# Kernel tuning notes

Hardware: AMD Instinct MI355X
Metric: run time of the kernel (lower is better)

The kernel has to match this reference:

```python
import jax, jax.numpy as jnp
import numpy as np

B, N, DIM, H, DH = 2, 256, 512, 8, 64
CLAMP = 40.0


def rmsnorm(x, w):
    eps = jnp.finfo(x.dtype).eps
    return x * jax.lax.rsqrt(jnp.mean(x * x, axis=-1, keepdims=True) + eps) * w


def strassen_attend(q, k1, k2, v1, v2, sim_clamp_value):
    # q,k1,k2: [b,h,n,d]; v1,v2: [b,h,n,dv]
    scale = q.shape[-1] ** -0.5
    q = q * scale
    sim1 = jnp.einsum('bhid,bhjd->bhij', q, k1)            # q . k1
    sim2 = jnp.einsum('bhid,bhkd->bhik', q, k2)            # q . k2
    sim3 = jnp.einsum('bhjd,bhkd->bhjk', k1, k2) * scale   # k1 . k2
    c = sim_clamp_value
    e1 = jnp.exp(jnp.clip(sim1, -c, c))
    e2 = jnp.exp(jnp.clip(sim2, -c, c))
    e3 = jnp.exp(jnp.clip(sim3, -c, c))
    # joint softmax over (j,k) of sim1[i,j]+sim2[i,k]+sim3[j,k], values v1[j]*v2[k]
    # factorized via exp(a+b+c)=exp(a)exp(b)exp(c):
    # D[b,h,i,j,d] = sum_k e2[i,k] e3[j,k] v2[k,d]
    D = jnp.einsum('bhik,bhjk,bhkd->bhijd', e2, e3, v2)
    num = jnp.einsum('bhij,bhjd,bhijd->bhid', e1, v1, D)
    den_ij = jnp.einsum('bhik,bhjk->bhij', e2, e3)
    den = jnp.einsum('bhij,bhij->bhi', e1, den_ij)
    return num / den[..., None]


def setup_inputs() -> dict:
    key = jax.random.key(0)
    k0, k1, k2 = jax.random.split(key, 3)
    x = jax.random.normal(k0, (B, N, DIM), dtype=jnp.float32)
    w_qkv = jax.random.normal(k1, (DIM, 5 * H * DH), dtype=jnp.float32) * (DIM ** -0.5)
    w_out = jax.random.normal(k2, (H * DH, DIM), dtype=jnp.float32) * ((H * DH) ** -0.5)
    q_norm_w = jnp.ones((DH,), jnp.float32)
    k1_norm_w = jnp.ones((DH,), jnp.float32)
    k2_norm_w = jnp.ones((DH,), jnp.float32)
    return {'x': x, 'w_qkv': w_qkv, 'w_out': w_out,
            'q_norm_w': q_norm_w, 'k1_norm_w': k1_norm_w, 'k2_norm_w': k2_norm_w}


def reference(x, w_qkv, w_out, q_norm_w, k1_norm_w, k2_norm_w):
    qkv = x @ w_qkv                                         # [b,n,5*h*d]
    q, k1, k2, v1, v2 = jnp.split(qkv, np.cumsum([H * DH] * 4), axis=-1)
    split_heads = lambda t: t.reshape(B, N, H, DH).transpose(0, 2, 1, 3)
    q, k1, k2, v1, v2 = map(split_heads, (q, k1, k2, v1, v2))
    q = rmsnorm(q, q_norm_w)
    k1 = rmsnorm(k1, k1_norm_w)
    k2 = rmsnorm(k2, k2_norm_w)
    out = strassen_attend(q, k1, k2, v1, v2, CLAMP)         # [b,h,n,d]
    out = out.transpose(0, 2, 1, 3).reshape(B, N, H * DH)
    return out @ w_out
```

## Files before the change

### kernel.cpp

```cpp
#include <hip/hip_runtime.h>
#include <hip/hip_bf16.h>


namespace {
constexpr int kN = 256, kH = 8, kDH = 64;
constexpr int kBH = 16;
constexpr int kBN = 512;
constexpr int kDIM = 512;
constexpr int kQKV = 2560;
constexpr float kEps = 1.1920928955078125e-07f;

typedef unsigned short u16;
typedef __attribute__((ext_vector_type(8))) short short8v;
typedef __attribute__((ext_vector_type(4))) float float4v;

constexpr size_t OF_XB   = 0;
constexpr size_t OF_WT   = OF_XB   + 131072;
constexpr size_t OF_WOT  = OF_WT   + 655360;
constexpr size_t OF_QKVB = OF_WOT  + 131072;
constexpr size_t OF_QB   = OF_QKVB + 655360;
constexpr size_t OF_K1B  = OF_QB   + 131072;
constexpr size_t OF_K2B  = OF_K1B  + 131072;
constexpr size_t OF_V1   = OF_K2B  + 131072;
constexpr size_t OF_V2T  = OF_V1   + 262144;
constexpr size_t OF_E1T  = OF_V2T  + 262144;
constexpr size_t OF_E2B  = OF_E1T  + 1048576;
constexpr size_t OF_E3F  = OF_E2B  + 524288;
constexpr size_t OF_NUM  = OF_E3F  + 524288;
constexpr size_t OF_DEN  = OF_NUM  + 262144;
constexpr size_t OF_ATNB = OF_DEN  + 4096;
}

__device__ __forceinline__ unsigned int bf16_rne(float a) {
  unsigned int u = __float_as_uint(a);
  return (u + 0x7fffu + ((u >> 16) & 1u)) >> 16;
}
__device__ __forceinline__ unsigned int pk2_bf16(float a, float b) {
  unsigned int ua = bf16_rne(a);
  unsigned int ub = __float_as_uint(b);
  ub = (ub + 0x7fffu + ((ub >> 16) & 1u)) & 0xffff0000u;
  return ua | ub;
}
__device__ __forceinline__ float bf2f(u16 v) {
  return __uint_as_float(((unsigned)v) << 16);
}

__global__ __launch_bounds__(256)
void conv_bf16(const float* __restrict__ in, u16* __restrict__ out) {
  const int id = blockIdx.x * 256 + threadIdx.x;
  float4 v = ((const float4*)in)[id];
  ushort4 o;
  o.x = (u16)bf16_rne(v.x); o.y = (u16)bf16_rne(v.y);
  o.z = (u16)bf16_rne(v.z); o.w = (u16)bf16_rne(v.w);
  ((ushort4*)out)[id] = o;
}

__global__ __launch_bounds__(256)
void transpose_bf16(const float* __restrict__ in, u16* __restrict__ out,
                    int rows, int cols) {
  __shared__ float tile[32][33];
  const int tx = threadIdx.x & 31, ty8 = threadIdx.x >> 5;
  const int c0 = blockIdx.x * 32, r0 = blockIdx.y * 32;
#pragma unroll
  for (int rr = 0; rr < 4; ++rr) {
    int r = ty8 + rr * 8;
    tile[r][tx] = in[(size_t)(r0 + r) * cols + c0 + tx];
  }
  __syncthreads();
#pragma unroll
  for (int rr = 0; rr < 4; ++rr) {
    int r = ty8 + rr * 8;
    out[(size_t)(c0 + r) * rows + r0 + tx] = (u16)bf16_rne(tile[tx][r]);
  }
}

template <bool F32OUT>
__global__ __launch_bounds__(256)
void gemm_mfma(const u16* __restrict__ A, const u16* __restrict__ BT,
               void* __restrict__ C, int M, int N, int K) {
  const int t = threadIdx.x, lane = t & 63, w = t >> 6;
  const int lrow = lane & 15, lk = lane >> 4;
  const int m0 = blockIdx.y * 64 + w * 16;
  const int n0 = blockIdx.x * 64;
  float4v acc[4] = {};
#pragma unroll 4
  for (int kk = 0; kk < K; kk += 32) {
    short8v aF = *(const short8v*)(A + (size_t)(m0 + lrow) * K + kk + lk * 8);
#pragma unroll
    for (int n = 0; n < 4; ++n) {
      short8v bF = *(const short8v*)(BT + (size_t)(n0 + n * 16 + lrow) * K + kk + lk * 8);
      acc[n] = __builtin_amdgcn_mfma_f32_16x16x32_bf16(aF, bF, acc[n], 0, 0, 0);
    }
  }
#pragma unroll
  for (int n = 0; n < 4; ++n)
#pragma unroll
    for (int r = 0; r < 4; ++r) {
      const int row = m0 + lk * 4 + r, col = n0 + n * 16 + lrow;
      if (F32OUT) ((float*)C)[(size_t)row * N + col] = acc[n][r];
      else        ((u16*)C)[(size_t)row * N + col] = (u16)bf16_rne(acc[n][r]);
    }
}

__global__ __launch_bounds__(64)
void rms_layout(const u16* __restrict__ qkvb,
                const float* __restrict__ wq, const float* __restrict__ wk1,
                const float* __restrict__ wk2,
                u16* __restrict__ Qb, u16* __restrict__ K1b,
                u16* __restrict__ K2b, float* __restrict__ V1,
                float* __restrict__ V2T) {
  const int bnh = blockIdx.x;
  const int h = bnh & 7;
  const int bn = bnh >> 3;
  const int b = bn >> 8;
  const int d = threadIdx.x;
  const u16* row = qkvb + (size_t)bn * kQKV;
  const int base = h * 64 + d;
  float q  = bf2f(row[0 * 512 + base]);
  float k1 = bf2f(row[1 * 512 + base]);
  float k2 = bf2f(row[2 * 512 + base]);
  float v1 = bf2f(row[3 * 512 + base]);
  float v2 = bf2f(row[4 * 512 + base]);
  float sq = q * q, s1 = k1 * k1, s2 = k2 * k2;
#pragma unroll
  for (int m = 32; m >= 1; m >>= 1) {
    sq += __shfl_xor(sq, m);
    s1 += __shfl_xor(s1, m);
    s2 += __shfl_xor(s2, m);
  }
  const float rq = rsqrtf(sq * (1.0f / 64) + kEps);
  const float r1 = rsqrtf(s1 * (1.0f / 64) + kEps);
  const float r2 = rsqrtf(s2 * (1.0f / 64) + kEps);
  const int bh = b * kH + h;
  const int n = bn & 255;
  const size_t o = ((size_t)bh * kN + n) * kDH + d;
  Qb[o]  = (u16)bf16_rne(q * rq * wq[d]);
  K1b[o] = (u16)bf16_rne(k1 * r1 * wk1[d]);
  K2b[o] = (u16)bf16_rne(k2 * r2 * wk2[d]);
  V1[o] = v1;
  V2T[((size_t)bh * kDH + d) * kN + n] = v2;
}

__global__ __launch_bounds__(256)
void sims_mfma(const u16* __restrict__ Qb, const u16* __restrict__ K1b,
               const u16* __restrict__ K2b, float* __restrict__ E1T,
               u16* __restrict__ E2b, u16* __restrict__ E3f) {
  __shared__ __align__(16) u16 Lt[64 * 80];
  const int bh = blockIdx.x, type = blockIdx.y;
  const int it = blockIdx.z >> 2, jt = blockIdx.z & 3;
  const int t = threadIdx.x, lane = t & 63, w = t >> 6;
  const int lrow = lane & 15, lk = lane >> 4;
  const u16* Ap = (type == 2 ? K1b : Qb) + (size_t)bh * 16384;
  const u16* Bp = (type == 0 ? K1b : K2b) + (size_t)bh * 16384;
  const int i0 = it * 64 + w * 16, j0 = jt * 64;
  float4v acc[4] = {};
#pragma unroll
  for (int kk = 0; kk < 2; ++kk) {
    short8v aF = *(const short8v*)(Ap + (size_t)(i0 + lrow) * 64 + kk * 32 + lk * 8);
#pragma unroll
    for (int n = 0; n < 4; ++n) {
      short8v bF = *(const short8v*)(Bp + (size_t)(j0 + n * 16 + lrow) * 64 + kk * 32 + lk * 8);
      acc[n] = __builtin_amdgcn_mfma_f32_16x16x32_bf16(aF, bF, acc[n], 0, 0, 0);
    }
  }
  if (type == 0) {
    float* Ep = E1T + (size_t)bh * 65536;
#pragma unroll
    for (int n = 0; n < 4; ++n)
#pragma unroll
      for (int r = 0; r < 4; ++r) {
        float s = acc[n][r] * 0.125f;
        s = fminf(fmaxf(s, -40.0f), 40.0f);
        Ep[(size_t)(j0 + n * 16 + lrow) * 256 + i0 + lk * 4 + r] = __expf(s);
      }
  } else if (type == 1) {
    u16* Ep = E2b + (size_t)bh * 65536;
#pragma unroll
    for (int n = 0; n < 4; ++n)
#pragma unroll
      for (int r = 0; r < 4; ++r) {
        float s = acc[n][r] * 0.125f;
        s = fminf(fmaxf(s, -40.0f), 40.0f);
        Ep[(size_t)(i0 + lk * 4 + r) * 256 + j0 + n * 16 + lrow] =
            (u16)bf16_rne(__expf(s));
      }
  } else {
#pragma unroll
    for (int n = 0; n < 4; ++n)
#pragma unroll
      for (int r = 0; r < 4; ++r) {
        float s = acc[n][r] * 0.125f;
        s = fminf(fmaxf(s, -40.0f), 40.0f);
        Lt[(w * 16 + lk * 4 + r) * 80 + n * 16 + lrow] = (u16)bf16_rne(__expf(s));
      }
    __syncthreads();
    u16* Ep = E3f + (size_t)bh * 65536;
#pragma unroll
    for (int ss = 0; ss < 2; ++ss) {
      const int sl = ss * 256 + t;
      const int nn = sl >> 7, sub = (sl >> 6) & 1, ln = sl & 63;
      const int lr = ln & 15, lq = ln >> 4;
      const uint4 v = *(const uint4*)&Lt[(nn * 16 + lr) * 80 + sub * 32 + lq * 8];
      const size_t gslot = (size_t)((((it * 4 + nn) * 4 + jt) * 2 + sub) * 64 + ln);
      *(uint4*)(Ep + gslot * 8) = v;
    }
  }
}

template <bool ISDEN>
__global__ __launch_bounds__(256)
void strassen_v3(const u16* __restrict__ E2b, const float* __restrict__ E1T,
                 const u16* __restrict__ E3f, const float* __restrict__ V1,
                 const float* __restrict__ V2T, float* __restrict__ NUM,
                 float* __restrict__ DEN) {
  constexpr int NDD = ISDEN ? 1 : 4;
  const int dblk = blockIdx.x;
  const int iblk = blockIdx.y;
  const int bh = blockIdx.z;
  const int d0 = dblk * 4;
  const int t = threadIdx.x;
  const int lane = t & 63, w = t >> 6;
  const int lrow = lane & 15, lk = lane >> 4;

  const size_t ebase = (size_t)bh * 65536;
  const u16* e2p = E2b + ebase;
  const float* e1p = E1T + ebase;
  const u16* e3p = E3f + ebase;
  const float* v2p = V2T + ((size_t)bh * kDH + d0) * kN;

  const int irowA = iblk * 64 + w * 16 + lrow;
  const int irowD = iblk * 64 + w * 16 + lk * 4;

  float p[NDD][4] = {};

#pragma unroll 1
  for (int ks = 0; ks < 4; ++ks) {
    short8v aFd[NDD][2];
#pragma unroll
    for (int sub = 0; sub < 2; ++sub) {
      const int kseg = ks * 64 + sub * 32 + lk * 8;
      const short8v araw = *(const short8v*)(e2p + (size_t)irowA * 256 + kseg);
      if (ISDEN) {
        aFd[0][sub] = araw;
      } else {
        float af[8];
#pragma unroll
        for (int e = 0; e < 8; ++e) af[e] = bf2f((u16)araw[e]);
#pragma unroll
        for (int dd = 0; dd < NDD; ++dd) {
          const float4 va = *(const float4*)(v2p + (size_t)dd * kN + kseg);
          const float4 vb = *(const float4*)(v2p + (size_t)dd * kN + kseg + 4);
          union { short8v s; uint4 u; } pk;
          pk.u.x = pk2_bf16(af[0] * va.x, af[1] * va.y);
          pk.u.y = pk2_bf16(af[2] * va.z, af[3] * va.w);
          pk.u.z = pk2_bf16(af[4] * vb.x, af[5] * vb.y);
          pk.u.w = pk2_bf16(af[6] * vb.z, af[7] * vb.w);
          aFd[dd][sub] = pk.s;
        }
      }
    }
#pragma unroll 2
    for (int jt = 0; jt < 4; ++jt) {
#pragma unroll
      for (int n = 0; n < 4; ++n) {
        float4v acc4[NDD] = {};
#pragma unroll
        for (int sub = 0; sub < 2; ++sub) {
          const short8v bF = *(const short8v*)(
              e3p + ((size_t)((((jt * 4 + n) * 4 + ks) * 2 + sub) * 64 + lane)) * 8);
#pragma unroll
          for (int dd = 0; dd < NDD; ++dd)
            acc4[dd] = __builtin_amdgcn_mfma_f32_16x16x32_bf16(
                aFd[dd][sub], bF, acc4[dd], 0, 0, 0);
        }
        const int j = jt * 64 + n * 16 + lrow;
        const float4 e4 = *(const float4*)(e1p + (size_t)j * 256 + irowD);
        const float e1f[4] = {e4.x, e4.y, e4.z, e4.w};
        if (ISDEN) {
#pragma unroll
          for (int r = 0; r < 4; ++r)
            p[0][r] = fmaf(e1f[r], acc4[0][r], p[0][r]);
        } else {
          const float4 v4 = *(const float4*)(V1 + ((size_t)bh * kN + j) * kDH + d0);
          const float v1s[4] = {v4.x, v4.y, v4.z, v4.w};
#pragma unroll
          for (int dd = 0; dd < NDD; ++dd)
#pragma unroll
            for (int r = 0; r < 4; ++r)
              p[dd][r] = fmaf(e1f[r] * v1s[dd], acc4[dd][r], p[dd][r]);
        }
      }
    }
  }

#pragma unroll
  for (int dd = 0; dd < NDD; ++dd)
#pragma unroll
    for (int r = 0; r < 4; ++r) {
      float v = p[dd][r];
      v += __shfl_xor(v, 1);
      v += __shfl_xor(v, 2);
      v += __shfl_xor(v, 4);
      v += __shfl_xor(v, 8);
      p[dd][r] = v;
    }
  if (lrow == 0) {
    if (!ISDEN) {
#pragma unroll
      for (int r = 0; r < 4; ++r)
#pragma unroll
        for (int dd = 0; dd < NDD; ++dd)
          NUM[((size_t)bh * kN + irowD + r) * kDH + d0 + dd] = p[dd][r];
    } else {
#pragma unroll
      for (int r = 0; r < 4; ++r)
        DEN[(size_t)bh * kN + irowD + r] = p[0][r];
    }
  }
}

__global__ __launch_bounds__(256)
void normalize_attn(const float* __restrict__ NUMp, const float* __restrict__ DENp,
                    u16* __restrict__ attnb) {
  const int idx = blockIdx.x * 256 + threadIdx.x;
  const int d = idx & 63;
  const int i = (idx >> 6) & 255;
  const int bh = idx >> 14;
  const int b = bh >> 3, h = bh & 7;
  const float v = NUMp[idx] / DENp[bh * kN + i];
  attnb[((size_t)(b * kN + i)) * kDIM + h * kDH + d] = (u16)bf16_rne(v);
}

extern "C" void kernel_launch(void* const* d_in, const int* in_sizes, int n_in,
                              void* d_out, int out_size, void* d_ws, size_t ws_size,
                              hipStream_t stream) {
  const float* x     = (const float*)d_in[0];
  const float* w_qkv = (const float*)d_in[1];
  const float* w_out = (const float*)d_in[2];
  const float* qw    = (const float*)d_in[3];
  const float* k1w   = (const float*)d_in[4];
  const float* k2w   = (const float*)d_in[5];

  float* ws = (float*)d_ws;
  u16* xb   = (u16*)(ws + OF_XB);
  u16* wT   = (u16*)(ws + OF_WT);
  u16* woT  = (u16*)(ws + OF_WOT);
  u16* qkvb = (u16*)(ws + OF_QKVB);
  u16* Qb   = (u16*)(ws + OF_QB);
  u16* K1b  = (u16*)(ws + OF_K1B);
  u16* K2b  = (u16*)(ws + OF_K2B);
  float* V1 = ws + OF_V1;
  float* V2T = ws + OF_V2T;
  float* E1T = ws + OF_E1T;
  u16* E2b  = (u16*)(ws + OF_E2B);
  u16* E3f  = (u16*)(ws + OF_E3F);
  float* NUMp = ws + OF_NUM;
  float* DENp = ws + OF_DEN;
  u16* atnb = (u16*)(ws + OF_ATNB);

  conv_bf16<<<dim3(kBN * kDIM / 1024), 256, 0, stream>>>(x, xb);
  transpose_bf16<<<dim3(kQKV / 32, kDIM / 32), 256, 0, stream>>>(
      w_qkv, wT, kDIM, kQKV);
  transpose_bf16<<<dim3(kDIM / 32, kDIM / 32), 256, 0, stream>>>(
      w_out, woT, kDIM, kDIM);

  gemm_mfma<false><<<dim3(kQKV / 64, kBN / 64), 256, 0, stream>>>(
      xb, wT, qkvb, kBN, kQKV, kDIM);

  rms_layout<<<dim3(kBN * kH), 64, 0, stream>>>(
      qkvb, qw, k1w, k2w, Qb, K1b, K2b, V1, V2T);

  sims_mfma<<<dim3(kBH, 3, 16), 256, 0, stream>>>(Qb, K1b, K2b, E1T, E2b, E3f);

  strassen_v3<false><<<dim3(16, 4, kBH), 256, 0, stream>>>(
      E2b, E1T, E3f, V1, V2T, NUMp, DENp);
  strassen_v3<true><<<dim3(1, 4, kBH), 256, 0, stream>>>(
      E2b, E1T, E3f, V1, V2T, NUMp, DENp);

  normalize_attn<<<dim3(1024), 256, 0, stream>>>(NUMp, DENp, atnb);

  gemm_mfma<true><<<dim3(kDIM / 64, kBN / 64), 256, 0, stream>>>(
      atnb, woT, d_out, kBN, kDIM, kDIM);
}
```

Baseline: 245.7 us.

## Split denominator into j-parallel kernel with atomics and widen numerator k-blocking

The denominator pass, previously 64 blocks each looping over all j and k, becomes a separate kernel that splits j across 4 blocks and combines partial sums with atomicAdd into a buffer zeroed by a memset. This is meant to shorten the serial denominator tail. The E3 fragment layout is reordered so one k-half's four fragments are contiguous. The numerator kernel now loops over two 128-wide k chunks with four MFMAs per accumulator chain, reducing outer iterations at the cost of more live registers. The atomics make the denominator sum order nondeterministic and add a memset launch.

```diff
diff --git a/kernel.cpp b/kernel.cpp
--- a/kernel.cpp
+++ b/kernel.cpp
@@ -201,19 +201,16 @@
       const int nn = sl >> 7, sub = (sl >> 6) & 1, ln = sl & 63;
       const int lr = ln & 15, lq = ln >> 4;
       const uint4 v = *(const uint4*)&Lt[(nn * 16 + lr) * 80 + sub * 32 + lq * 8];
-      const size_t gslot = (size_t)((((it * 4 + nn) * 4 + jt) * 2 + sub) * 64 + ln);
+      const size_t gslot = (size_t)(((it * 4 + nn) * 8 + jt * 2 + sub) * 64 + ln);
       *(uint4*)(Ep + gslot * 8) = v;
     }
   }
 }
 
-template <bool ISDEN>
-__global__ __launch_bounds__(256)
-void strassen_v3(const u16* __restrict__ E2b, const float* __restrict__ E1T,
+__global__ __launch_bounds__(256)
+void strassen_v4(const u16* __restrict__ E2b, const float* __restrict__ E1T,
                  const u16* __restrict__ E3f, const float* __restrict__ V1,
-                 const float* __restrict__ V2T, float* __restrict__ NUM,
-                 float* __restrict__ DEN) {
-  constexpr int NDD = ISDEN ? 1 : 4;
+                 const float* __restrict__ V2T, float* __restrict__ NUM) {
   const int dblk = blockIdx.x;
   const int iblk = blockIdx.y;
   const int bh = blockIdx.z;
@@ -227,74 +224,69 @@
   const float* e1p = E1T + ebase;
   const u16* e3p = E3f + ebase;
   const float* v2p = V2T + ((size_t)bh * kDH + d0) * kN;
+  const float* v1p = V1 + (size_t)bh * kN * kDH + d0;
 
   const int irowA = iblk * 64 + w * 16 + lrow;
   const int irowD = iblk * 64 + w * 16 + lk * 4;
 
-  float p[NDD][4] = {};
+  float p[4][4] = {};
 
 #pragma unroll 1
-  for (int ks = 0; ks < 4; ++ks) {
-    short8v aFd[NDD][2];
-#pragma unroll
-    for (int sub = 0; sub < 2; ++sub) {
-      const int kseg = ks * 64 + sub * 32 + lk * 8;
+  for (int kso = 0; kso < 2; ++kso) {
+    const int kbase = kso * 128;
+    short8v aFd[4][4];
+#pragma unroll
+    for (int s = 0; s < 4; ++s) {
+      const int kseg = kbase + s * 32 + lk * 8;
       const short8v araw = *(const short8v*)(e2p + (size_t)irowA * 256 + kseg);
-      if (ISDEN) {
-        aFd[0][sub] = araw;
-      } else {
-        float af[8];
-#pragma unroll
-        for (int e = 0; e < 8; ++e) af[e] = bf2f((u16)araw[e]);
-#pragma unroll
-        for (int dd = 0; dd < NDD; ++dd) {
-          const float4 va = *(const float4*)(v2p + (size_t)dd * kN + kseg);
-          const float4 vb = *(const float4*)(v2p + (size_t)dd * kN + kseg + 4);
-          union { short8v s; uint4 u; } pk;
-          pk.u.x = pk2_bf16(af[0] * va.x, af[1] * va.y);
-          pk.u.y = pk2_bf16(af[2] * va.z, af[3] * va.w);
-          pk.u.z = pk2_bf16(af[4] * vb.x, af[5] * vb.y);
-          pk.u.w = pk2_bf16(af[6] * vb.z, af[7] * vb.w);
-          aFd[dd][sub] = pk.s;
-        }
+      float af[8];
+#pragma unroll
+      for (int e = 0; e < 8; ++e) af[e] = bf2f((u16)araw[e]);
+#pragma unroll
+      for (int dd = 0; dd < 4; ++dd) {
+        const float4 va = *(const float4*)(v2p + (size_t)dd * kN + kseg);
+        const float4 vb = *(const float4*)(v2p + (size_t)dd * kN + kseg + 4);
+        union { short8v s8; uint4 u; } pk;
+        pk.u.x = pk2_bf16(af[0] * va.x, af[1] * va.y);
+        pk.u.y = pk2_bf16(af[2] * va.z, af[3] * va.w);
+        pk.u.z = pk2_bf16(af[4] * vb.x, af[5] * vb.y);
+        pk.u.w = pk2_bf16(af[6] * vb.z, af[7] * vb.w);
+        aFd[dd][s] = pk.s8;
       }
     }
 #pragma unroll 2
     for (int jt = 0; jt < 4; ++jt) {
 #pragma unroll
       for (int n = 0; n < 4; ++n) {
-        float4v acc4[NDD] = {};
-#pragma unroll
-        for (int sub = 0; sub < 2; ++sub) {
-          const short8v bF = *(const short8v*)(
-              e3p + ((size_t)((((jt * 4 + n) * 4 + ks) * 2 + sub) * 64 + lane)) * 8);
-#pragma unroll
-          for (int dd = 0; dd < NDD; ++dd)
-            acc4[dd] = __builtin_amdgcn_mfma_f32_16x16x32_bf16(
-                aFd[dd][sub], bF, acc4[dd], 0, 0, 0);
+        const u16* bb = e3p + ((size_t)((jt * 4 + n) * 8 + kso * 4) * 64 + lane) * 8;
+        const short8v bF0 = *(const short8v*)(bb + 0 * 512);
+        const short8v bF1 = *(const short8v*)(bb + 1 * 512);
+        const short8v bF2 = *(const short8v*)(bb + 2 * 512);
+        const short8v bF3 = *(const short8v*)(bb + 3 * 512);
+        float4v acc4[4] = {};
+#pragma unroll
+        for (int dd = 0; dd < 4; ++dd) {
+          acc4[dd] = __builtin_amdgcn_mfma_f32_16x16x32_bf16(aFd[dd][0], bF0, acc4[dd], 0, 0, 0);
+          acc4[dd] = __builtin_amdgcn_mfma_f32_16x16x32_bf16(aFd[dd][1], bF1, acc4[dd], 0, 0, 0);
+          acc4[dd] = __builtin_amdgcn_mfma_f32_16x16x32_bf16(aFd[dd][2], bF2, acc4[dd], 0, 0, 0);
+          acc4[dd] = __builtin_amdgcn_mfma_f32_16x16x32_bf16(aFd[dd][3], bF3, acc4[dd], 0, 0, 0);
         }
         const int j = jt * 64 + n * 16 + lrow;
         const float4 e4 = *(const float4*)(e1p + (size_t)j * 256 + irowD);
+        const float4 v4 = *(const float4*)(v1p + (size_t)j * kDH);
         const float e1f[4] = {e4.x, e4.y, e4.z, e4.w};
-        if (ISDEN) {
+        const float v1s[4] = {v4.x, v4.y, v4.z, v4.w};
+#pragma unroll
+        for (int dd = 0; dd < 4; ++dd)
 #pragma unroll
           for (int r = 0; r < 4; ++r)
-            p[0][r] = fmaf(e1f[r], acc4[0][r], p[0][r]);
-        } else {
-          const float4 v4 = *(const float4*)(V1 + ((size_t)bh * kN + j) * kDH + d0);
-          const float v1s[4] = {v4.x, v4.y, v4.z, v4.w};
-#pragma unroll
-          for (int dd = 0; dd < NDD; ++dd)
-#pragma unroll
-            for (int r = 0; r < 4; ++r)
-              p[dd][r] = fmaf(e1f[r] * v1s[dd], acc4[dd][r], p[dd][r]);
-        }
+            p[dd][r] = fmaf(e1f[r] * v1s[dd], acc4[dd][r], p[dd][r]);
       }
     }
   }
 
 #pragma unroll
-  for (int dd = 0; dd < NDD; ++dd)
+  for (int dd = 0; dd < 4; ++dd)
 #pragma unroll
     for (int r = 0; r < 4; ++r) {
       float v = p[dd][r];
@@ -305,17 +297,65 @@
       p[dd][r] = v;
     }
   if (lrow == 0) {
-    if (!ISDEN) {
-#pragma unroll
-      for (int r = 0; r < 4; ++r)
-#pragma unroll
-        for (int dd = 0; dd < NDD; ++dd)
-          NUM[((size_t)bh * kN + irowD + r) * kDH + d0 + dd] = p[dd][r];
-    } else {
-#pragma unroll
-      for (int r = 0; r < 4; ++r)
-        DEN[(size_t)bh * kN + irowD + r] = p[0][r];
-    }
+#pragma unroll
+    for (int r = 0; r < 4; ++r)
+#pragma unroll
+      for (int dd = 0; dd < 4; ++dd)
+        NUM[((size_t)bh * kN + irowD + r) * kDH + d0 + dd] = p[dd][r];
+  }
+}
+
+__global__ __launch_bounds__(256)
+void strassen_den(const u16* __restrict__ E2b, const float* __restrict__ E1T,
+                  const u16* __restrict__ E3f, float* __restrict__ DEN) {
+  const int jblk = blockIdx.x;
+  const int iblk = blockIdx.y;
+  const int bh = blockIdx.z;
+  const int t = threadIdx.x;
+  const int lane = t & 63, w = t >> 6;
+  const int lrow = lane & 15, lk = lane >> 4;
+
+  const size_t ebase = (size_t)bh * 65536;
+  const u16* e2p = E2b + ebase;
+  const float* e1p = E1T + ebase;
+  const u16* e3p = E3f + ebase;
+  const int irowA = iblk * 64 + w * 16 + lrow;
+  const int irowD = iblk * 64 + w * 16 + lk * 4;
+
+  float4v acc[4] = {};
+#pragma unroll
+  for (int s = 0; s < 8; ++s) {
+    const short8v aF = *(const short8v*)(e2p + (size_t)irowA * 256 + s * 32 + lk * 8);
+#pragma unroll
+    for (int n = 0; n < 4; ++n) {
+      const short8v bF = *(const short8v*)(
+          e3p + ((size_t)(((jblk * 4 + n) * 8 + s) * 64 + lane)) * 8);
+      acc[n] = __builtin_amdgcn_mfma_f32_16x16x32_bf16(aF, bF, acc[n], 0, 0, 0);
+    }
+  }
+  float p[4] = {};
+#pragma unroll
+  for (int n = 0; n < 4; ++n) {
+    const int j = jblk * 64 + n * 16 + lrow;
+    const float4 e4 = *(const float4*)(e1p + (size_t)j * 256 + irowD);
+    p[0] = fmaf(e4.x, acc[n][0], p[0]);
+    p[1] = fmaf(e4.y, acc[n][1], p[1]);
+    p[2] = fmaf(e4.z, acc[n][2], p[2]);
+    p[3] = fmaf(e4.w, acc[n][3], p[3]);
+  }
+#pragma unroll
+  for (int r = 0; r < 4; ++r) {
+    float v = p[r];
+    v += __shfl_xor(v, 1);
+    v += __shfl_xor(v, 2);
+    v += __shfl_xor(v, 4);
+    v += __shfl_xor(v, 8);
+    p[r] = v;
+  }
+  if (lrow == 0) {
+#pragma unroll
+    for (int r = 0; r < 4; ++r)
+      atomicAdd(&DEN[(size_t)bh * kN + irowD + r], p[r]);
   }
 }
 
@@ -358,6 +398,8 @@
   float* DENp = ws + OF_DEN;
   u16* atnb = (u16*)(ws + OF_ATNB);
 
+  hipMemsetAsync(DENp, 0, 4096 * sizeof(float), stream);
+
   conv_bf16<<<dim3(kBN * kDIM / 1024), 256, 0, stream>>>(x, xb);
   transpose_bf16<<<dim3(kQKV / 32, kDIM / 32), 256, 0, stream>>>(
       w_qkv, wT, kDIM, kQKV);
@@ -372,10 +414,9 @@
 
   sims_mfma<<<dim3(kBH, 3, 16), 256, 0, stream>>>(Qb, K1b, K2b, E1T, E2b, E3f);
 
-  strassen_v3<false><<<dim3(16, 4, kBH), 256, 0, stream>>>(
-      E2b, E1T, E3f, V1, V2T, NUMp, DENp);
-  strassen_v3<true><<<dim3(1, 4, kBH), 256, 0, stream>>>(
-      E2b, E1T, E3f, V1, V2T, NUMp, DENp);
+  strassen_den<<<dim3(4, 4, kBH), 256, 0, stream>>>(E2b, E1T, E3f, DENp);
+  strassen_v4<<<dim3(16, 4, kBH), 256, 0, stream>>>(
+      E2b, E1T, E3f, V1, V2T, NUMp);
 
   normalize_attn<<<dim3(1024), 256, 0, stream>>>(NUMp, DENp, atnb);
 
```

Result: faster. 199.2 us (-18.9%).
